# Performance work log

Hardware: AMD Instinct MI355X
Metric: run time of the kernel (lower is better)

## Reference

```python
import jax, jax.numpy as jnp
import numpy as np

B, L, C = 32, 128, 20
TOKEN_EMBED, VOC_IV, VOC_OOEV = 300, 100000, 20000
CHAR_EMBED, CHAR_SIZE = 50, 100
NUM_FILTERS, KERNEL = 200, 3
LABELS, HID = 8, 256
NS = 6  # B,I,E,S,O,EOS states per CRF


def _lstm_dir(x, mask, w_ih, w_hh, b, reverse):
    # x: [B,L,D], mask: [B,L] -> [B,L,H]
    Bb = x.shape[0]
    Hh = w_hh.shape[1]
    xs = jnp.einsum('bld,gd->blg', x, w_ih) + b  # precompute input part [B,L,4H]
    xs_t = jnp.swapaxes(xs, 0, 1)   # [L,B,4H]
    m_t = jnp.swapaxes(mask, 0, 1)  # [L,B]
    h0 = jnp.zeros((Bb, Hh), x.dtype)

    def step(carry, inp):
        h, c = carry
        gx, m = inp
        gates = gx + h @ w_hh.T
        i, f, g, o = jnp.split(gates, 4, axis=-1)
        i = jax.nn.sigmoid(i); f = jax.nn.sigmoid(f)
        g = jnp.tanh(g); o = jax.nn.sigmoid(o)
        c_new = f * c + i * g
        h_new = o * jnp.tanh(c_new)
        mm = m[:, None]
        h = mm * h_new + (1.0 - mm) * h
        c = mm * c_new + (1.0 - mm) * c
        return (h, c), h

    _, hs = jax.lax.scan(step, (h0, h0), (xs_t, m_t), reverse=reverse)
    return jnp.swapaxes(hs, 0, 1)


def _bilstm(x, mask, layer_params):
    for (w_ih, w_hh, b) in layer_params:
        fwd = _lstm_dir(x, mask, w_ih[0], w_hh[0], b[0], False)
        bwd = _lstm_dir(x, mask, w_ih[1], w_hh[1], b[1], True)
        x = jnp.concatenate([fwd, bwd], axis=-1)
    return x


def _crf_loss(em, trans, target, mask):
    # em: [B,L,NS], trans: [NS,NS], target: [B,L] -> scalar NLL summed over batch
    em_y = jnp.take_along_axis(em, target[:, :, None], axis=2)[:, :, 0]
    tr_y = trans[target[:, :-1], target[:, 1:]]
    score = jnp.sum(em_y * mask, axis=1) + jnp.sum(tr_y * mask[:, 1:], axis=1)
    em_t = jnp.swapaxes(em, 0, 1)   # [L,B,NS]
    m_t = jnp.swapaxes(mask, 0, 1)
    alpha0 = em_t[0]

    def step(alpha, inp):
        e, m = inp
        new = jax.nn.logsumexp(alpha[:, :, None] + trans[None, :, :], axis=1) + e
        alpha = m[:, None] * new + (1.0 - m[:, None]) * alpha
        return alpha, None

    alpha, _ = jax.lax.scan(step, alpha0, (em_t[1:], m_t[1:]))
    logZ = jax.nn.logsumexp(alpha, axis=1)
    return jnp.sum(logZ - score)


def setup_inputs() -> dict:
    key = jax.random.key(0)
    ks = jax.random.split(key, 20)
    D0 = TOKEN_EMBED + NUM_FILTERS      # 500: BiLSTM layer-0 input
    D1 = 2 * HID                        # 512: BiLSTM layer-1 input
    s = 0.05
    return {
        'input_word_iv': jax.random.randint(ks[0], (B, L), 0, VOC_IV),
        'input_word_ooev': jax.random.randint(ks[1], (B, L), 0, VOC_OOEV),
        'input_char': jax.random.randint(ks[2], (B, L, C), 0, CHAR_SIZE),
        'target': jax.random.randint(ks[3], (LABELS, B, L), 0, NS),
        'mask': jnp.ones((B, L), jnp.float32),
        'embedd_word': jax.random.normal(ks[4], (VOC_IV, TOKEN_EMBED), jnp.float32) * s,
        'ooev_table': jax.random.normal(ks[5], (VOC_OOEV, TOKEN_EMBED), jnp.float32) * s,
        'char_table': jax.random.normal(ks[6], (CHAR_SIZE, CHAR_EMBED), jnp.float32) * s,
        'conv_w': jax.random.normal(ks[7], (NUM_FILTERS, CHAR_EMBED, KERNEL), jnp.float32) * s,
        'conv_b': jnp.zeros((NUM_FILTERS,), jnp.float32),
        'w_ih0': jax.random.normal(ks[8], (2, 4 * HID, D0), jnp.float32) * s,
        'w_hh0': jax.random.normal(ks[9], (2, 4 * HID, HID), jnp.float32) * s,
        'b0': jnp.zeros((2, 4 * HID), jnp.float32),
        'w_ih1': jax.random.normal(ks[10], (2, 4 * HID, D1), jnp.float32) * s,
        'w_hh1': jax.random.normal(ks[11], (2, 4 * HID, HID), jnp.float32) * s,
        'b1': jnp.zeros((2, 4 * HID), jnp.float32),
        'crf_w': jax.random.normal(ks[12], (LABELS, D1, NS), jnp.float32) * s,
        'crf_b': jnp.zeros((LABELS, NS), jnp.float32),
        'crf_trans': jax.random.normal(ks[13], (LABELS, NS, NS), jnp.float32) * s,
    }


def reference(input_word_iv, input_word_ooev, input_char, target, mask,
              embedd_word, ooev_table, char_table, conv_w, conv_b,
              w_ih0, w_hh0, b0, w_ih1, w_hh1, b1,
              crf_w, crf_b, crf_trans):
    # word embedding: frozen iv table + masked OOEV correction
    word = embedd_word[input_word_iv] \
        + (input_word_ooev != 0).astype(jnp.float32)[:, :, None] * ooev_table[input_word_ooev]
    # char CNN: masked embed -> conv1d (pad k-1 both sides) -> max-over-time -> sigmoid
    ch = (input_char != 0).astype(jnp.float32)[..., None] * char_table[input_char]  # [B,L,C,E]
    ch = ch.reshape(B * L, C, CHAR_EMBED).transpose(0, 2, 1)  # [B*L,E,C]
    conv = jax.lax.conv_general_dilated(ch, conv_w, (1,), [(KERNEL - 1, KERNEL - 1)],
                                        dimension_numbers=('NCH', 'OIH', 'NCH'))
    conv = conv + conv_b[None, :, None]
    char_feat = jax.nn.sigmoid(jnp.max(conv, axis=2)).reshape(B, L, NUM_FILTERS)
    inp = jnp.concatenate([word, char_feat], axis=2)  # [B,L,500]
    out = _bilstm(inp, mask, [(w_ih0, w_hh0, b0), (w_ih1, w_hh1, b1)])  # [B,L,512]
    # per-label CRF emissions [K,B,L,NS]
    em = jnp.einsum('bld,kdn->kbln', out, crf_w) + crf_b[:, None, None, :]
    losses = jax.vmap(_crf_loss, in_axes=(0, 0, 0, None))(em, crf_trans, target, mask)
    return jnp.sum(losses) / B
```

## Files before the change

### kernel.cpp

```cpp
#include <hip/hip_runtime.h>
#include <hip/hip_bf16.h>


typedef float floatx2 __attribute__((ext_vector_type(2)));
typedef short bf16x8 __attribute__((ext_vector_type(8)));
typedef float f32x4  __attribute__((ext_vector_type(4)));

__device__ __forceinline__ unsigned short f2bf(float x) {
    unsigned u = __float_as_uint(x);
    unsigned r = (u + 0x7fffu + ((u >> 16) & 1u)) >> 16;
    return (unsigned short)r;
}

__device__ __forceinline__ void pk_fma_bl(floatx2& acc, floatx2 w, floatx2 h) {
    asm("v_pk_fma_f32 %0, %1, %2, %0 op_sel_hi:[1,0,1]" : "+v"(acc) : "v"(w), "v"(h));
}
__device__ __forceinline__ void pk_fma_bh(floatx2& acc, floatx2 w, floatx2 h) {
    asm("v_pk_fma_f32 %0, %1, %2, %0 op_sel:[0,1,0]" : "+v"(acc) : "v"(w), "v"(h));
}

__device__ __forceinline__ float fsig(float x) {
    return __builtin_amdgcn_rcpf(1.f + __expf(-x));
}
__device__ __forceinline__ float ftanh(float x) {
    return fmaf(-2.f, __builtin_amdgcn_rcpf(1.f + __expf(2.f * x)), 1.f);
}

__device__ __forceinline__ void dot4(floatx2& aif0, floatx2& ago0,
                                     floatx2& aif1, floatx2& ago1,
                                     uint4 w, const float* hsp, int k4) {
    float4 hv = *(const float4*)(hsp + k4 * 4);
    floatx2 h01; h01.x = hv.x; h01.y = hv.y;
    floatx2 h23; h23.x = hv.z; h23.y = hv.w;
    floatx2 lo, hi;
    lo = __builtin_amdgcn_cvt_pk_f32_fp8((int)w.x, false);
    hi = __builtin_amdgcn_cvt_pk_f32_fp8((int)w.x, true);
    pk_fma_bl(aif0, lo, h01); pk_fma_bl(ago0, hi, h01);
    lo = __builtin_amdgcn_cvt_pk_f32_fp8((int)w.y, false);
    hi = __builtin_amdgcn_cvt_pk_f32_fp8((int)w.y, true);
    pk_fma_bh(aif0, lo, h01); pk_fma_bh(ago0, hi, h01);
    lo = __builtin_amdgcn_cvt_pk_f32_fp8((int)w.z, false);
    hi = __builtin_amdgcn_cvt_pk_f32_fp8((int)w.z, true);
    pk_fma_bl(aif1, lo, h23); pk_fma_bl(ago1, hi, h23);
    lo = __builtin_amdgcn_cvt_pk_f32_fp8((int)w.w, false);
    hi = __builtin_amdgcn_cvt_pk_f32_fp8((int)w.w, true);
    pk_fma_bh(aif1, lo, h23); pk_fma_bh(ago1, hi, h23);
}

__global__ void prep(const float* __restrict__ wh0, const float* __restrict__ wh1,
                     const float* __restrict__ crf_w, const float* __restrict__ conv_w,
                     unsigned* __restrict__ Wp0, unsigned* __restrict__ Wp1,
                     float* __restrict__ crfBT, float* __restrict__ convWT,
                     float* __restrict__ outp)
{
    int idx = blockIdx.x * 256 + threadIdx.x;
    if (idx == 0) outp[0] = 0.f;
    const int NWP = 2 * 2 * 128 * 256;
    if (idx < NWP) {
        int layer = idx >> 16;
        int r     = idx & 65535;
        int dir   = r >> 15;
        int q     = r & 32767;
        int k2    = q >> 8;
        int t     = q & 255;
        const float* w = (layer ? wh1 : wh0) + dir * 1024 * 256;
        unsigned vx, vy;
        {
            int k = 2 * k2;
            float wi = w[(t      ) * 256 + k];
            float wf = w[(256 + t) * 256 + k];
            float wg = w[(512 + t) * 256 + k];
            float wo = w[(768 + t) * 256 + k];
            int u = __builtin_amdgcn_cvt_pk_fp8_f32(wi, wf, 0, false);
            u     = __builtin_amdgcn_cvt_pk_fp8_f32(wg, wo, u, true);
            vx = (unsigned)u;
        }
        {
            int k = 2 * k2 + 1;
            float wi = w[(t      ) * 256 + k];
            float wf = w[(256 + t) * 256 + k];
            float wg = w[(512 + t) * 256 + k];
            float wo = w[(768 + t) * 256 + k];
            int u = __builtin_amdgcn_cvt_pk_fp8_f32(wi, wf, 0, false);
            u     = __builtin_amdgcn_cvt_pk_fp8_f32(wg, wo, u, true);
            vy = (unsigned)u;
        }
        unsigned* dst = layer ? Wp1 : Wp0;
        int k4 = k2 >> 1, half = k2 & 1;
        size_t e = ((((size_t)dir * 64 + k4) * 256) + t) * 4 + half * 2;
        dst[e]     = vx;
        dst[e + 1] = vy;
        return;
    }
    idx -= NWP;
    if (idx < 48 * 512) {
        int jj = idx >> 9, d = idx & 511;
        int kL = jj / 6, n = jj % 6;
        crfBT[idx] = crf_w[(kL * 512 + d) * 6 + n];
        return;
    }
    idx -= 48 * 512;
    if (idx < 30000) {
        int f = idx % 200, ek = idx / 200;
        int e = ek / 3, kk = ek % 3;
        convWT[idx] = conv_w[(f * 50 + e) * 3 + kk];
        return;
    }
}

__global__ __launch_bounds__(256) void embed_conv(
    const int* __restrict__ iv, const int* __restrict__ ov, const int* __restrict__ ch,
    const float* __restrict__ emb, const float* __restrict__ ooev, const float* __restrict__ ctab,
    const float* __restrict__ convWT, const float* __restrict__ convB,
    float* __restrict__ inp)
{
    const int bl = blockIdx.x;
    const int tid = threadIdx.x;
    __shared__ float sx[50 * 20];
    const int ivv = iv[bl];
    const int ovv = ov[bl];
    const float mo = (ovv != 0) ? 1.f : 0.f;
    for (int e = tid; e < 300; e += 256)
        inp[bl * 500 + e] = emb[(size_t)ivv * 300 + e] + mo * ooev[(size_t)ovv * 300 + e];
    for (int i = tid; i < 1000; i += 256) {
        int cI = i / 50, e = i % 50;
        int id = ch[bl * 20 + cI];
        sx[e * 20 + cI] = id ? ctab[id * 50 + e] : 0.f;
    }
    __syncthreads();
    if (tid < 200) {
        float acc[22];
        float bz = convB[tid];
        #pragma unroll
        for (int o = 0; o < 22; ++o) acc[o] = bz;
        for (int e = 0; e < 50; ++e) {
            float xr[20];
            #pragma unroll
            for (int q = 0; q < 5; ++q) {
                float4 v = *(const float4*)&sx[e * 20 + q * 4];
                xr[q * 4 + 0] = v.x; xr[q * 4 + 1] = v.y;
                xr[q * 4 + 2] = v.z; xr[q * 4 + 3] = v.w;
            }
            float w0 = convWT[(e * 3 + 0) * 200 + tid];
            float w1 = convWT[(e * 3 + 1) * 200 + tid];
            float w2 = convWT[(e * 3 + 2) * 200 + tid];
            #pragma unroll
            for (int o = 0; o < 22; ++o) {
                float s = acc[o];
                if (o >= 2)            s = fmaf(xr[o - 2], w0, s);
                if (o >= 1 && o <= 20) s = fmaf(xr[o - 1], w1, s);
                if (o <= 19)           s = fmaf(xr[o],     w2, s);
                acc[o] = s;
            }
        }
        float mx = acc[0];
        #pragma unroll
        for (int o = 1; o < 22; ++o) mx = fmaxf(mx, acc[o]);
        inp[bl * 500 + 300 + tid] = 1.f / (1.f + expf(-mx));
    }
}

__global__ __launch_bounds__(256) void gemm_mfma(
    const float* __restrict__ A, const float* __restrict__ Bm,
    const float* __restrict__ bias, float* __restrict__ C,
    int M, int N, int K)
{
    __shared__ unsigned short As[4][128][8];
    __shared__ unsigned short Bs[4][128][8];
    const int tid  = threadIdx.x;
    const int wave = tid >> 6, lane = tid & 63;
    const int quad = lane >> 4, lr = lane & 15;
    const int m0 = blockIdx.y * 128, n0 = blockIdx.x * 128;

    f32x4 acc[2][8];
    #pragma unroll
    for (int mt = 0; mt < 2; ++mt)
        #pragma unroll
        for (int nt = 0; nt < 8; ++nt) acc[mt][nt] = (f32x4){0.f, 0.f, 0.f, 0.f};

    const int ktiles = (K + 31) >> 5;
    for (int kt = 0; kt < ktiles; ++kt) {
        #pragma unroll
        for (int i = 0; i < 4; ++i) {
            int vid = tid + i * 256;
            int row = vid >> 3, kq = vid & 7;
            int kb  = kt * 32 + kq * 4;
            unsigned short ta[4], tb[4];
            const float* pa = A  + (size_t)(m0 + row) * K + kb;
            const float* pb = Bm + (size_t)(n0 + row) * K + kb;
            #pragma unroll
            for (int j = 0; j < 4; ++j) {
                ta[j] = (kb + j < K) ? f2bf(pa[j]) : (unsigned short)0;
                tb[j] = (kb + j < K) ? f2bf(pb[j]) : (unsigned short)0;
            }
            int ko = kq >> 1, jo = (kq & 1) * 4;
            *(ushort4*)&As[ko][row][jo] = make_ushort4(ta[0], ta[1], ta[2], ta[3]);
            *(ushort4*)&Bs[ko][row][jo] = make_ushort4(tb[0], tb[1], tb[2], tb[3]);
        }
        __syncthreads();
        bf16x8 bfr[8];
        #pragma unroll
        for (int nt = 0; nt < 8; ++nt)
            bfr[nt] = *(const bf16x8*)&Bs[quad][nt * 16 + lr][0];
        #pragma unroll
        for (int mt = 0; mt < 2; ++mt) {
            bf16x8 afr = *(const bf16x8*)&As[quad][wave * 32 + mt * 16 + lr][0];
            #pragma unroll
            for (int nt = 0; nt < 8; ++nt)
                acc[mt][nt] = __builtin_amdgcn_mfma_f32_16x16x32_bf16(
                    afr, bfr[nt], acc[mt][nt], 0, 0, 0);
        }
        __syncthreads();
    }
    #pragma unroll
    for (int mt = 0; mt < 2; ++mt)
        #pragma unroll
        for (int r = 0; r < 4; ++r) {
            int m = m0 + wave * 32 + mt * 16 + quad * 4 + r;
            #pragma unroll
            for (int nt = 0; nt < 8; ++nt) {
                int n = n0 + nt * 16 + lr;
                C[(size_t)m * N + n] = acc[mt][nt][r] + bias[n];
            }
        }
}

__global__ __launch_bounds__(256) void gemm_bt(
    const float* __restrict__ A, const float* __restrict__ Bm,
    const float* __restrict__ bias, float* __restrict__ C,
    int M, int N, int K)
{
    __shared__ float At[16 * 128];
    __shared__ float Bt[16 * 128];
    const int tid = threadIdx.x;
    const int tx = tid & 15, ty = tid >> 4;
    const int m0 = blockIdx.y * 128, n0 = blockIdx.x * 128;
    float acc[2][2][4][4];
    #pragma unroll
    for (int a = 0; a < 2; ++a)
        #pragma unroll
        for (int b = 0; b < 2; ++b)
            #pragma unroll
            for (int i = 0; i < 4; ++i)
                #pragma unroll
                for (int j = 0; j < 4; ++j) acc[a][b][i][j] = 0.f;

    const int lr = tid >> 2;
    const int lc = (tid & 3) << 2;
    const int ktiles = (K + 15) >> 4;
    for (int kt = 0; kt < ktiles; ++kt) {
        const int k0 = kt << 4;
        #pragma unroll
        for (int half = 0; half < 2; ++half) {
            int r = lr + half * 64;
            int gk = k0 + lc;
            {
                int gm = m0 + r;
                float4 v = make_float4(0.f, 0.f, 0.f, 0.f);
                if (gm < M) {
                    const float* p = A + (size_t)gm * K + gk;
                    if (gk + 3 < K) v = *(const float4*)p;
                    else {
                        if (gk + 0 < K) v.x = p[0];
                        if (gk + 1 < K) v.y = p[1];
                        if (gk + 2 < K) v.z = p[2];
                        if (gk + 3 < K) v.w = p[3];
                    }
                }
                At[(lc + 0) * 128 + r] = v.x; At[(lc + 1) * 128 + r] = v.y;
                At[(lc + 2) * 128 + r] = v.z; At[(lc + 3) * 128 + r] = v.w;
            }
            {
                int gn = n0 + r;
                float4 v = make_float4(0.f, 0.f, 0.f, 0.f);
                if (gn < N) {
                    const float* p = Bm + (size_t)gn * K + gk;
                    if (gk + 3 < K) v = *(const float4*)p;
                    else {
                        if (gk + 0 < K) v.x = p[0];
                        if (gk + 1 < K) v.y = p[1];
                        if (gk + 2 < K) v.z = p[2];
                        if (gk + 3 < K) v.w = p[3];
                    }
                }
                Bt[(lc + 0) * 128 + r] = v.x; Bt[(lc + 1) * 128 + r] = v.y;
                Bt[(lc + 2) * 128 + r] = v.z; Bt[(lc + 3) * 128 + r] = v.w;
            }
        }
        __syncthreads();
        #pragma unroll
        for (int k = 0; k < 16; ++k) {
            float4 a0 = *(const float4*)&At[k * 128 + (ty << 2)];
            float4 a1 = *(const float4*)&At[k * 128 + 64 + (ty << 2)];
            float4 b0 = *(const float4*)&Bt[k * 128 + (tx << 2)];
            float4 b1 = *(const float4*)&Bt[k * 128 + 64 + (tx << 2)];
            float am[2][4] = {{a0.x, a0.y, a0.z, a0.w}, {a1.x, a1.y, a1.z, a1.w}};
            float bn[2][4] = {{b0.x, b0.y, b0.z, b0.w}, {b1.x, b1.y, b1.z, b1.w}};
            #pragma unroll
            for (int qa = 0; qa < 2; ++qa)
                #pragma unroll
                for (int qb = 0; qb < 2; ++qb)
                    #pragma unroll
                    for (int i = 0; i < 4; ++i)
                        #pragma unroll
                        for (int j = 0; j < 4; ++j)
                            acc[qa][qb][i][j] = fmaf(am[qa][i], bn[qb][j], acc[qa][qb][i][j]);
        }
        __syncthreads();
    }
    #pragma unroll
    for (int qa = 0; qa < 2; ++qa)
        #pragma unroll
        for (int i = 0; i < 4; ++i) {
            int m = m0 + qa * 64 + (ty << 2) + i;
            if (m >= M) continue;
            #pragma unroll
            for (int qb = 0; qb < 2; ++qb)
                #pragma unroll
                for (int j = 0; j < 4; ++j) {
                    int n = n0 + qb * 64 + (tx << 2) + j;
                    if (n < N) C[(size_t)m * N + n] = acc[qa][qb][i][j] + bias[n];
                }
        }
}

#define L4LDS 36
__global__ __launch_bounds__(1024) void lstm_rec(
    const float* __restrict__ xs, const uint4* __restrict__ Wp,
    const float* __restrict__ mask, float* __restrict__ out)
{
    const int tid = threadIdx.x;
    const int t   = tid & 255;
    const int kh  = tid >> 8;
    const int b   = blockIdx.x >> 1;
    const int dir = blockIdx.x & 1;
    __shared__ uint4 wlds[L4LDS * 256];
    __shared__ float4 part[3 * 256];
    __shared__ __align__(16) float hs[256];
    __shared__ float msk[128];

    const uint4* wp = Wp + (size_t)dir * 64 * 256;
    for (int j = tid; j < L4LDS * 256; j += 1024) wlds[j] = wp[j];
    if (tid < 256) hs[tid] = 0.f;
    if (tid < 128) msk[tid] = mask[b * 128 + tid];
    __syncthreads();

    const uint4* sp = wp + t;
    float h = 0.f, c = 0.f;
    for (int s = 0; s < 128; ++s) {
        const int l = dir ? (127 - s) : s;
        floatx2 aif0 = {0.f, 0.f}, ago0 = {0.f, 0.f};
        floatx2 aif1 = {0.f, 0.f}, ago1 = {0.f, 0.f};
        float gi, gf, gg2, go;
        if (kh == 0) {
            const float* gxp = xs + ((size_t)(b * 128 + l) * 2048 + dir * 1024 + t);
            gi = gxp[0]; gf = gxp[256]; gg2 = gxp[512]; go = gxp[768];
            #pragma unroll 4
            for (int k4 = 0; k4 < 13; ++k4)
                dot4(aif0, ago0, aif1, ago1, wlds[k4 * 256 + t], hs, k4);
        } else if (kh == 1) {
            uint4 a0 = sp[36 * 256], a1 = sp[37 * 256];
            uint4 a2 = sp[38 * 256], a3 = sp[39 * 256];
            #pragma unroll 4
            for (int k4 = 13; k4 < 27; ++k4)
                dot4(aif0, ago0, aif1, ago1, wlds[k4 * 256 + t], hs, k4);
            dot4(aif0, ago0, aif1, ago1, a0, hs, 36);
            dot4(aif0, ago0, aif1, ago1, a1, hs, 37);
            dot4(aif0, ago0, aif1, ago1, a2, hs, 38);
            dot4(aif0, ago0, aif1, ago1, a3, hs, 39);
        } else if (kh == 2) {
            uint4 a0 = sp[40 * 256], a1 = sp[41 * 256];
            uint4 a2 = sp[42 * 256], a3 = sp[43 * 256];
            uint4 b0 = sp[44 * 256], b1 = sp[45 * 256];
            uint4 b2 = sp[46 * 256], b3 = sp[47 * 256];
            #pragma unroll 3
            for (int k4 = 27; k4 < 36; ++k4)
                dot4(aif0, ago0, aif1, ago1, wlds[k4 * 256 + t], hs, k4);
            dot4(aif0, ago0, aif1, ago1, a0, hs, 40);
            dot4(aif0, ago0, aif1, ago1, a1, hs, 41);
            dot4(aif0, ago0, aif1, ago1, a2, hs, 42);
            dot4(aif0, ago0, aif1, ago1, a3, hs, 43);
            dot4(aif0, ago0, aif1, ago1, b0, hs, 44);
            dot4(aif0, ago0, aif1, ago1, b1, hs, 45);
            dot4(aif0, ago0, aif1, ago1, b2, hs, 46);
            dot4(aif0, ago0, aif1, ago1, b3, hs, 47);
        } else {
            uint4 a0 = sp[48 * 256], a1 = sp[49 * 256];
            uint4 a2 = sp[50 * 256], a3 = sp[51 * 256];
            uint4 b0 = sp[52 * 256], b1 = sp[53 * 256];
            uint4 b2 = sp[54 * 256], b3 = sp[55 * 256];
            dot4(aif0, ago0, aif1, ago1, a0, hs, 48);
            dot4(aif0, ago0, aif1, ago1, a1, hs, 49);
            dot4(aif0, ago0, aif1, ago1, a2, hs, 50);
            dot4(aif0, ago0, aif1, ago1, a3, hs, 51);
            a0 = sp[56 * 256]; a1 = sp[57 * 256];
            a2 = sp[58 * 256]; a3 = sp[59 * 256];
            dot4(aif0, ago0, aif1, ago1, b0, hs, 52);
            dot4(aif0, ago0, aif1, ago1, b1, hs, 53);
            dot4(aif0, ago0, aif1, ago1, b2, hs, 54);
            dot4(aif0, ago0, aif1, ago1, b3, hs, 55);
            b0 = sp[60 * 256]; b1 = sp[61 * 256];
            b2 = sp[62 * 256]; b3 = sp[63 * 256];
            dot4(aif0, ago0, aif1, ago1, a0, hs, 56);
            dot4(aif0, ago0, aif1, ago1, a1, hs, 57);
            dot4(aif0, ago0, aif1, ago1, a2, hs, 58);
            dot4(aif0, ago0, aif1, ago1, a3, hs, 59);
            dot4(aif0, ago0, aif1, ago1, b0, hs, 60);
            dot4(aif0, ago0, aif1, ago1, b1, hs, 61);
            dot4(aif0, ago0, aif1, ago1, b2, hs, 62);
            dot4(aif0, ago0, aif1, ago1, b3, hs, 63);
        }
        floatx2 aif = aif0 + aif1;
        floatx2 ago = ago0 + ago1;
        if (kh != 0)
            part[(kh - 1) * 256 + t] = make_float4(aif.x, aif.y, ago.x, ago.y);
        __syncthreads();
        if (kh == 0) {
            float4 p0 = part[t], p1 = part[256 + t], p2 = part[512 + t];
            float sai = aif.x + gi  + p0.x + p1.x + p2.x;
            float saf = aif.y + gf  + p0.y + p1.y + p2.y;
            float sag = ago.x + gg2 + p0.z + p1.z + p2.z;
            float sao = ago.y + go  + p0.w + p1.w + p2.w;
            float ig = fsig(sai);
            float fg = fsig(saf);
            float og = fsig(sao);
            float gg = ftanh(sag);
            float cn = fmaf(fg, c, ig * gg);
            float hn = og * ftanh(cn);
            float m = msk[l];
            h = m * hn + (1.f - m) * h;
            c = m * cn + (1.f - m) * c;
            hs[t] = h;
            out[(size_t)(b * 128 + l) * 512 + dir * 256 + t] = h;
        }
        __syncthreads();
    }
}
#undef L4LDS

__global__ __launch_bounds__(192) void crf_loss(
    const float* __restrict__ em, const float* __restrict__ trans,
    const int* __restrict__ target, const float* __restrict__ mask,
    float* __restrict__ outp)
{
    const int k = blockIdx.x;
    const int tid = threadIdx.x;
    const int b = tid & 31;
    const int j = tid >> 5;
    __shared__ float T[36];
    __shared__ float As[32][6];
    __shared__ float red[192];
    if (tid < 36) T[tid] = trans[k * 36 + tid];
    __syncthreads();
    const int* tg = target + (k * 32 + b) * 128;
    float sc = 0.f;
    for (int l = j; l < 128; l += 6) {
        int y = tg[l];
        float m = mask[b * 128 + l];
        sc += m * em[(b * 128 + l) * 48 + k * 6 + y];
        if (l > 0) sc += m * T[tg[l - 1] * 6 + y];
    }
    red[tid] = sc;
    float a = em[(b * 128) * 48 + k * 6 + j];
    As[b][j] = a;
    __syncthreads();
    for (int l = 1; l < 128; ++l) {
        float e = em[(b * 128 + l) * 48 + k * 6 + j];
        float v0 = As[b][0] + T[0 * 6 + j];
        float v1 = As[b][1] + T[1 * 6 + j];
        float v2 = As[b][2] + T[2 * 6 + j];
        float v3 = As[b][3] + T[3 * 6 + j];
        float v4 = As[b][4] + T[4 * 6 + j];
        float v5 = As[b][5] + T[5 * 6 + j];
        float mx = fmaxf(fmaxf(fmaxf(v0, v1), fmaxf(v2, v3)), fmaxf(v4, v5));
        float ssum = expf(v0 - mx) + expf(v1 - mx) + expf(v2 - mx)
                   + expf(v3 - mx) + expf(v4 - mx) + expf(v5 - mx);
        float na = mx + logf(ssum) + e;
        float m = mask[b * 128 + l];
        a = m * na + (1.f - m) * a;
        __syncthreads();
        As[b][j] = a;
        __syncthreads();
    }
    if (j == 0) {
        float v0 = As[b][0], v1 = As[b][1], v2 = As[b][2];
        float v3 = As[b][3], v4 = As[b][4], v5 = As[b][5];
        float mx = fmaxf(fmaxf(fmaxf(v0, v1), fmaxf(v2, v3)), fmaxf(v4, v5));
        float ssum = expf(v0 - mx) + expf(v1 - mx) + expf(v2 - mx)
                   + expf(v3 - mx) + expf(v4 - mx) + expf(v5 - mx);
        float logZ = mx + logf(ssum);
        float scb = red[b] + red[b + 32] + red[b + 64] + red[b + 96] + red[b + 128] + red[b + 160];
        red[b] = logZ - scb;
    }
    __syncthreads();
    if (tid == 0) {
        float tot = 0.f;
        for (int bb = 0; bb < 32; ++bb) tot += red[bb];
        atomicAdd(outp, tot * (1.f / 32.f));
    }
}

extern "C" void kernel_launch(void* const* d_in, const int* in_sizes, int n_in,
                              void* d_out, int out_size, void* d_ws, size_t ws_size,
                              hipStream_t stream)
{
    const int*   iv    = (const int*)d_in[0];
    const int*   ov    = (const int*)d_in[1];
    const int*   ch    = (const int*)d_in[2];
    const int*   tgt   = (const int*)d_in[3];
    const float* mask  = (const float*)d_in[4];
    const float* emb   = (const float*)d_in[5];
    const float* ooevT = (const float*)d_in[6];
    const float* ctab  = (const float*)d_in[7];
    const float* convW = (const float*)d_in[8];
    const float* convB = (const float*)d_in[9];
    const float* wih0  = (const float*)d_in[10];
    const float* whh0  = (const float*)d_in[11];
    const float* b0    = (const float*)d_in[12];
    const float* wih1  = (const float*)d_in[13];
    const float* whh1  = (const float*)d_in[14];
    const float* b1    = (const float*)d_in[15];
    const float* crfW  = (const float*)d_in[16];
    const float* crfB  = (const float*)d_in[17];
    const float* crfT  = (const float*)d_in[18];
    float* outp = (float*)d_out;

    char* ws = (char*)d_ws;
    size_t off = 0;
    auto alloc = [&](size_t bytes) {
        void* p = ws + off;
        off = (off + bytes + 255) & ~(size_t)255;
        return p;
    };
    float* inp    = (float*)alloc((size_t)4096 * 500 * 4);
    float* xs     = (float*)alloc((size_t)4096 * 2048 * 4);
    float* out0   = (float*)alloc((size_t)4096 * 512 * 4);
    float* out1   = (float*)alloc((size_t)4096 * 512 * 4);
    float* em     = (float*)alloc((size_t)4096 * 48 * 4);
    unsigned* Wp0 = (unsigned*)alloc((size_t)2 * 128 * 256 * 8);
    unsigned* Wp1 = (unsigned*)alloc((size_t)2 * 128 * 256 * 8);
    float* crfBT  = (float*)alloc((size_t)48 * 512 * 4);
    float* convWT = (float*)alloc((size_t)30000 * 4);

    const int prepN = 2 * 2 * 128 * 256 + 48 * 512 + 30000;
    prep<<<(prepN + 255) / 256, 256, 0, stream>>>(whh0, whh1, crfW, convW,
                                                  Wp0, Wp1, crfBT, convWT, outp);
    embed_conv<<<4096, 256, 0, stream>>>(iv, ov, ch, emb, ooevT, ctab, convWT, convB, inp);
    gemm_mfma<<<dim3(16, 32), 256, 0, stream>>>(inp, wih0, b0, xs, 4096, 2048, 500);
    lstm_rec<<<64, 1024, 0, stream>>>(xs, (const uint4*)Wp0, mask, out0);
    gemm_mfma<<<dim3(16, 32), 256, 0, stream>>>(out0, wih1, b1, xs, 4096, 2048, 512);
    lstm_rec<<<64, 1024, 0, stream>>>(xs, (const uint4*)Wp1, mask, out1);
    gemm_bt<<<dim3(1, 32), 256, 0, stream>>>(out1, crfBT, crfB, em, 4096, 48, 512);
    crf_loss<<<8, 192, 0, stream>>>(em, crfT, tgt, mask, outp);
}
```

Before: 1.325 ms.

## Pre-convert GEMM operands to padded bf16 and tile the recurrent weight repack

Activations and input-projection weights are now converted to bf16 once, either in a prep kernel or at the producer (embed_conv and lstm_rec write a bf16 copy). K is padded to 512 so the GEMM loads 16-byte bf16 vectors straight into LDS, with no per-element fp32 loads, conversions or bounds checks. The W_hh fp8 repack moves to a separate LDS-tiled kernel that writes uint4s with coalesced accesses. In exchange the change adds extra conversion passes over the weights, extra bf16 output writes from the LSTM, and more workspace.

```diff
diff --git a/kernel.cpp b/kernel.cpp
--- a/kernel.cpp
+++ b/kernel.cpp
@@ -47,52 +47,26 @@
     pk_fma_bh(aif1, lo, h23); pk_fma_bh(ago1, hi, h23);
 }
 
-__global__ void prep(const float* __restrict__ wh0, const float* __restrict__ wh1,
-                     const float* __restrict__ crf_w, const float* __restrict__ conv_w,
-                     unsigned* __restrict__ Wp0, unsigned* __restrict__ Wp1,
-                     float* __restrict__ crfBT, float* __restrict__ convWT,
-                     float* __restrict__ outp)
+__global__ void prep_misc(const float* __restrict__ wih0, const float* __restrict__ wih1,
+                          const float* __restrict__ crf_w, const float* __restrict__ conv_w,
+                          unsigned short* __restrict__ wbf0, unsigned short* __restrict__ wbf1,
+                          float* __restrict__ crfBT, float* __restrict__ convWT,
+                          float* __restrict__ outp)
 {
     int idx = blockIdx.x * 256 + threadIdx.x;
     if (idx == 0) outp[0] = 0.f;
-    const int NWP = 2 * 2 * 128 * 256;
-    if (idx < NWP) {
-        int layer = idx >> 16;
-        int r     = idx & 65535;
-        int dir   = r >> 15;
-        int q     = r & 32767;
-        int k2    = q >> 8;
-        int t     = q & 255;
-        const float* w = (layer ? wh1 : wh0) + dir * 1024 * 256;
-        unsigned vx, vy;
-        {
-            int k = 2 * k2;
-            float wi = w[(t      ) * 256 + k];
-            float wf = w[(256 + t) * 256 + k];
-            float wg = w[(512 + t) * 256 + k];
-            float wo = w[(768 + t) * 256 + k];
-            int u = __builtin_amdgcn_cvt_pk_fp8_f32(wi, wf, 0, false);
-            u     = __builtin_amdgcn_cvt_pk_fp8_f32(wg, wo, u, true);
-            vx = (unsigned)u;
-        }
-        {
-            int k = 2 * k2 + 1;
-            float wi = w[(t      ) * 256 + k];
-            float wf = w[(256 + t) * 256 + k];
-            float wg = w[(512 + t) * 256 + k];
-            float wo = w[(768 + t) * 256 + k];
-            int u = __builtin_amdgcn_cvt_pk_fp8_f32(wi, wf, 0, false);
-            u     = __builtin_amdgcn_cvt_pk_fp8_f32(wg, wo, u, true);
-            vy = (unsigned)u;
-        }
-        unsigned* dst = layer ? Wp1 : Wp0;
-        int k4 = k2 >> 1, half = k2 & 1;
-        size_t e = ((((size_t)dir * 64 + k4) * 256) + t) * 4 + half * 2;
-        dst[e]     = vx;
-        dst[e + 1] = vy;
+    const int NW = 2048 * 512;
+    if (idx < NW) {
+        int n = idx >> 9, k = idx & 511;
+        wbf0[idx] = (k < 500) ? f2bf(wih0[n * 500 + k]) : (unsigned short)0;
         return;
     }
-    idx -= NWP;
+    idx -= NW;
+    if (idx < NW) {
+        wbf1[idx] = f2bf(wih1[idx]);
+        return;
+    }
+    idx -= NW;
     if (idx < 48 * 512) {
         int jj = idx >> 9, d = idx & 511;
         int kL = jj / 6, n = jj % 6;
@@ -108,11 +82,56 @@
     }
 }
 
+__global__ __launch_bounds__(256) void prep_whh(
+    const float* __restrict__ wh0, const float* __restrict__ wh1,
+    uint4* __restrict__ Wp0, uint4* __restrict__ Wp1)
+{
+    const int bid   = blockIdx.x;
+    const int layer = bid >> 5;
+    const int dir   = (bid >> 4) & 1;
+    const int tt    = (bid >> 2) & 3;
+    const int ktile = bid & 3;
+    const float* w = (layer ? wh1 : wh0) + dir * 1024 * 256;
+    uint4* dst = layer ? Wp1 : Wp0;
+    const int t0 = tt * 64, k0 = ktile * 64;
+    __shared__ float sxw[4][64][65];
+    const int tid = threadIdx.x;
+    #pragma unroll
+    for (int g = 0; g < 4; ++g)
+        #pragma unroll
+        for (int q = 0; q < 4; ++q) {
+            int lin = q * 256 + tid;
+            int tr = lin >> 4, kc = (lin & 15) * 4;
+            float4 v = *(const float4*)&w[(g * 256 + t0 + tr) * 256 + k0 + kc];
+            sxw[g][tr][kc + 0] = v.x; sxw[g][tr][kc + 1] = v.y;
+            sxw[g][tr][kc + 2] = v.z; sxw[g][tr][kc + 3] = v.w;
+        }
+    __syncthreads();
+    const int t = tid & 63, k4g = tid >> 6;
+    #pragma unroll
+    for (int q = 0; q < 4; ++q) {
+        int k4l = k4g * 4 + q;
+        unsigned wrd[4];
+        #pragma unroll
+        for (int j = 0; j < 4; ++j) {
+            int kc = k4l * 4 + j;
+            float wi = sxw[0][t][kc], wf = sxw[1][t][kc];
+            float wg = sxw[2][t][kc], wo = sxw[3][t][kc];
+            int u = __builtin_amdgcn_cvt_pk_fp8_f32(wi, wf, 0, false);
+            u     = __builtin_amdgcn_cvt_pk_fp8_f32(wg, wo, u, true);
+            wrd[j] = (unsigned)u;
+        }
+        int k4 = (k0 >> 2) + k4l;
+        dst[((size_t)dir * 64 + k4) * 256 + (t0 + t)] =
+            make_uint4(wrd[0], wrd[1], wrd[2], wrd[3]);
+    }
+}
+
 __global__ __launch_bounds__(256) void embed_conv(
     const int* __restrict__ iv, const int* __restrict__ ov, const int* __restrict__ ch,
     const float* __restrict__ emb, const float* __restrict__ ooev, const float* __restrict__ ctab,
     const float* __restrict__ convWT, const float* __restrict__ convB,
-    float* __restrict__ inp)
+    unsigned short* __restrict__ inp)
 {
     const int bl = blockIdx.x;
     const int tid = threadIdx.x;
@@ -121,12 +140,13 @@
     const int ovv = ov[bl];
     const float mo = (ovv != 0) ? 1.f : 0.f;
     for (int e = tid; e < 300; e += 256)
-        inp[bl * 500 + e] = emb[(size_t)ivv * 300 + e] + mo * ooev[(size_t)ovv * 300 + e];
+        inp[bl * 512 + e] = f2bf(emb[(size_t)ivv * 300 + e] + mo * ooev[(size_t)ovv * 300 + e]);
     for (int i = tid; i < 1000; i += 256) {
         int cI = i / 50, e = i % 50;
         int id = ch[bl * 20 + cI];
         sx[e * 20 + cI] = id ? ctab[id * 50 + e] : 0.f;
     }
+    if (tid >= 200 && tid < 212) inp[bl * 512 + 300 + tid] = 0;
     __syncthreads();
     if (tid < 200) {
         float acc[22];
@@ -156,14 +176,13 @@
         float mx = acc[0];
         #pragma unroll
         for (int o = 1; o < 22; ++o) mx = fmaxf(mx, acc[o]);
-        inp[bl * 500 + 300 + tid] = 1.f / (1.f + expf(-mx));
-    }
-}
-
-__global__ __launch_bounds__(256) void gemm_mfma(
-    const float* __restrict__ A, const float* __restrict__ Bm,
-    const float* __restrict__ bias, float* __restrict__ C,
-    int M, int N, int K)
+        inp[bl * 512 + 300 + tid] = f2bf(1.f / (1.f + expf(-mx)));
+    }
+}
+
+__global__ __launch_bounds__(256) void gemm_bf16(
+    const unsigned short* __restrict__ A, const unsigned short* __restrict__ Bm,
+    const float* __restrict__ bias, float* __restrict__ C, int N)
 {
     __shared__ unsigned short As[4][128][8];
     __shared__ unsigned short Bs[4][128][8];
@@ -178,24 +197,15 @@
         #pragma unroll
         for (int nt = 0; nt < 8; ++nt) acc[mt][nt] = (f32x4){0.f, 0.f, 0.f, 0.f};
 
-    const int ktiles = (K + 31) >> 5;
-    for (int kt = 0; kt < ktiles; ++kt) {
-        #pragma unroll
-        for (int i = 0; i < 4; ++i) {
-            int vid = tid + i * 256;
-            int row = vid >> 3, kq = vid & 7;
-            int kb  = kt * 32 + kq * 4;
-            unsigned short ta[4], tb[4];
-            const float* pa = A  + (size_t)(m0 + row) * K + kb;
-            const float* pb = Bm + (size_t)(n0 + row) * K + kb;
-            #pragma unroll
-            for (int j = 0; j < 4; ++j) {
-                ta[j] = (kb + j < K) ? f2bf(pa[j]) : (unsigned short)0;
-                tb[j] = (kb + j < K) ? f2bf(pb[j]) : (unsigned short)0;
-            }
-            int ko = kq >> 1, jo = (kq & 1) * 4;
-            *(ushort4*)&As[ko][row][jo] = make_ushort4(ta[0], ta[1], ta[2], ta[3]);
-            *(ushort4*)&Bs[ko][row][jo] = make_ushort4(tb[0], tb[1], tb[2], tb[3]);
+    for (int kt = 0; kt < 16; ++kt) {
+        #pragma unroll
+        for (int p = 0; p < 2; ++p) {
+            int lin = p * 256 + tid;
+            int row = lin & 127, c = lin >> 7;
+            *(bf16x8*)&As[c][row][0] =
+                *(const bf16x8*)&A[(size_t)(m0 + row) * 512 + kt * 32 + c * 8];
+            *(bf16x8*)&Bs[c][row][0] =
+                *(const bf16x8*)&Bm[(size_t)(n0 + row) * 512 + kt * 32 + c * 8];
         }
         __syncthreads();
         bf16x8 bfr[8];
@@ -327,7 +337,8 @@
 #define L4LDS 36
 __global__ __launch_bounds__(1024) void lstm_rec(
     const float* __restrict__ xs, const uint4* __restrict__ Wp,
-    const float* __restrict__ mask, float* __restrict__ out)
+    const float* __restrict__ mask, float* __restrict__ out,
+    unsigned short* __restrict__ outb)
 {
     const int tid = threadIdx.x;
     const int t   = tid & 255;
@@ -431,7 +442,9 @@
             h = m * hn + (1.f - m) * h;
             c = m * cn + (1.f - m) * c;
             hs[t] = h;
-            out[(size_t)(b * 128 + l) * 512 + dir * 256 + t] = h;
+            size_t oi = (size_t)(b * 128 + l) * 512 + dir * 256 + t;
+            out[oi]  = h;
+            outb[oi] = f2bf(h);
         }
         __syncthreads();
     }
@@ -532,24 +545,29 @@
         off = (off + bytes + 255) & ~(size_t)255;
         return p;
     };
-    float* inp    = (float*)alloc((size_t)4096 * 500 * 4);
+    unsigned short* inp_bf = (unsigned short*)alloc((size_t)4096 * 512 * 2);
     float* xs     = (float*)alloc((size_t)4096 * 2048 * 4);
     float* out0   = (float*)alloc((size_t)4096 * 512 * 4);
     float* out1   = (float*)alloc((size_t)4096 * 512 * 4);
+    unsigned short* outb0 = (unsigned short*)alloc((size_t)4096 * 512 * 2);
+    unsigned short* outb1 = (unsigned short*)alloc((size_t)4096 * 512 * 2);
     float* em     = (float*)alloc((size_t)4096 * 48 * 4);
-    unsigned* Wp0 = (unsigned*)alloc((size_t)2 * 128 * 256 * 8);
-    unsigned* Wp1 = (unsigned*)alloc((size_t)2 * 128 * 256 * 8);
+    uint4* Wp0    = (uint4*)alloc((size_t)2 * 64 * 256 * 16);
+    uint4* Wp1    = (uint4*)alloc((size_t)2 * 64 * 256 * 16);
+    unsigned short* wbf0 = (unsigned short*)alloc((size_t)2048 * 512 * 2);
+    unsigned short* wbf1 = (unsigned short*)alloc((size_t)2048 * 512 * 2);
     float* crfBT  = (float*)alloc((size_t)48 * 512 * 4);
     float* convWT = (float*)alloc((size_t)30000 * 4);
 
-    const int prepN = 2 * 2 * 128 * 256 + 48 * 512 + 30000;
-    prep<<<(prepN + 255) / 256, 256, 0, stream>>>(whh0, whh1, crfW, convW,
-                                                  Wp0, Wp1, crfBT, convWT, outp);
-    embed_conv<<<4096, 256, 0, stream>>>(iv, ov, ch, emb, ooevT, ctab, convWT, convB, inp);
-    gemm_mfma<<<dim3(16, 32), 256, 0, stream>>>(inp, wih0, b0, xs, 4096, 2048, 500);
-    lstm_rec<<<64, 1024, 0, stream>>>(xs, (const uint4*)Wp0, mask, out0);
-    gemm_mfma<<<dim3(16, 32), 256, 0, stream>>>(out0, wih1, b1, xs, 4096, 2048, 512);
-    lstm_rec<<<64, 1024, 0, stream>>>(xs, (const uint4*)Wp1, mask, out1);
+    const int miscN = 2 * 2048 * 512 + 48 * 512 + 30000;
+    prep_misc<<<(miscN + 255) / 256, 256, 0, stream>>>(wih0, wih1, crfW, convW,
+                                                       wbf0, wbf1, crfBT, convWT, outp);
+    prep_whh<<<64, 256, 0, stream>>>(whh0, whh1, Wp0, Wp1);
+    embed_conv<<<4096, 256, 0, stream>>>(iv, ov, ch, emb, ooevT, ctab, convWT, convB, inp_bf);
+    gemm_bf16<<<dim3(16, 32), 256, 0, stream>>>(inp_bf, wbf0, b0, xs, 2048);
+    lstm_rec<<<64, 1024, 0, stream>>>(xs, Wp0, mask, out0, outb0);
+    gemm_bf16<<<dim3(16, 32), 256, 0, stream>>>(outb0, wbf1, b1, xs, 2048);
+    lstm_rec<<<64, 1024, 0, stream>>>(xs, Wp1, mask, out1, outb1);
     gemm_bt<<<dim3(1, 32), 256, 0, stream>>>(out1, crfBT, crfB, em, 4096, 48, 512);
     crf_loss<<<8, 192, 0, stream>>>(em, crfT, tgt, mask, outp);
 }
```

Measured after the change: 1.188 ms. 1.12x faster.
